# Kernel tuning notes

Hardware: AMD Instinct MI355X
Metric: run time of the kernel (lower is better)

The kernel has to match this reference:

```python
import jax, jax.numpy as jnp
import numpy as np

NEURONS = 512
CHANNELS = 384
H, W = 13, 13
BATCH = 512


def setup_inputs() -> dict:
    key = jax.random.key(0)
    kx, ks, kd, kb = jax.random.split(key, 4)
    x = jax.random.normal(kx, (BATCH, CHANNELS, H, W), dtype=jnp.float32)
    W_s = jax.random.normal(ks, (NEURONS, H, W), dtype=jnp.float32)      # spatial readout per neuron
    W_d = jax.random.normal(kd, (NEURONS, CHANNELS), dtype=jnp.float32)  # channel readout (squeezed 1x1 conv kernel)
    W_b = jax.random.normal(kb, (1, NEURONS), dtype=jnp.float32)
    return {"x": x, "W_s": W_s, "W_d": W_d, "W_b": W_b}


def reference(x, W_s, W_d, W_b):
    # Original: out = einsum('bchw,nhw->bnchw') -> per-neuron 1x1 conv with W_d[n] -> sum over (c,h,w) -> + W_b
    # Mathematically: out[b,n] = sum_{c,h,w} x[b,c,h,w] * W_s[n,h,w] * W_d[n,c] + W_b[0,n]
    # Factorized into two contractions, avoiding the (b,n,c,h,w) intermediate.
    pooled = jnp.einsum('bchw,nhw->bnc', x, W_s)   # spatial weighted pooling: [B, N, C]
    out = jnp.einsum('bnc,nc->bn', pooled, W_d)    # channel readout: [B, N]
    return out + W_b
```

## Files before the change

### kernel.cpp

```cpp
#include <hip/hip_runtime.h>


#define B_   512
#define C_   384
#define N_   512
#define HW_  169
#define CT   128
#define SXR  200
#define RSTR 520

#define WSF_ELEMS  ((size_t)32 * 6 * 64 * 8)
#define WDF_ELEMS  ((size_t)24 * 32 * 64 * 4)
#define PART_ELEMS ((size_t)3 * B_ * N_)

typedef __bf16 bf16x8 __attribute__((ext_vector_type(8)));
typedef float f32x4  __attribute__((ext_vector_type(4)));
typedef float f32x4u __attribute__((ext_vector_type(4), aligned(4)));
typedef unsigned u32x4 __attribute__((ext_vector_type(4)));

__device__ __forceinline__ __bf16 f2bf(float f) {
  union { float f; unsigned u; } v; v.f = f;
  unsigned r = (v.u + 0x7FFFu + ((v.u >> 16) & 1u)) >> 16;
  unsigned short s = (unsigned short)r;
  return __builtin_bit_cast(__bf16, s);
}

__device__ __forceinline__ unsigned pack_trunc(float a, float b) {
  return __builtin_amdgcn_perm(__builtin_bit_cast(unsigned, b),
                               __builtin_bit_cast(unsigned, a), 0x07060302u);
}

__global__ __launch_bounds__(256)
void prep_aux_kernel(const float* __restrict__ Ws,
                     const float* __restrict__ Wd,
                     __bf16* __restrict__ wsf,
                     float* __restrict__ wdf) {
  int t = blockIdx.x * 256 + threadIdx.x;
  if (t < 12288) {
    int lane = t & 63;
    int fr   = t >> 6;
    int kb   = fr % 6;
    int nm   = fr / 6;
    int n    = nm * 16 + (lane & 15);
    int k0   = kb * 32 + (lane >> 4) * 8;
    const float* src = Ws + (size_t)n * HW_;
    bf16x8 v;
    #pragma unroll
    for (int j = 0; j < 8; ++j) {
      int k = k0 + j;
      float f = (k < HW_) ? src[k] : 0.f;
      v[j] = f2bf(f);
    }
    *(bf16x8*)(wsf + (size_t)t * 8) = v;
  } else {
    int t2 = t - 12288;
    int lane = t2 & 63;
    int fr   = t2 >> 6;
    int nm   = fr & 31;
    int cm   = fr >> 5;
    int n    = nm * 16 + (lane & 15);
    int c0   = cm * 16 + (lane >> 4) * 4;
    f32x4 w = *(const f32x4u*)(Wd + (size_t)n * C_ + c0);
    *(f32x4*)(wdf + (size_t)t2 * 4) = w;
  }
}

__global__ __launch_bounds__(256, 4)
void conv_part(const float* __restrict__ x,
               const __bf16* __restrict__ wsf,
               const float* __restrict__ wdf,
               float* __restrict__ part) {
  __shared__ float red[16 * RSTR];

  const int tid  = threadIdx.x;
  const int id    = blockIdx.x;
  const int slot  = id & 7;
  const int t8    = id >> 3;
  const int c_blk = t8 % 3;
  const int b     = (t8 / 3) * 8 + slot;

  const int lane  = tid & 63;
  const int wv    = tid >> 6;
  const int lrow  = lane & 15;
  const int lquad = lane >> 4;

  bf16x8 a[2][6];
  #pragma unroll
  for (int mi = 0; mi < 2; ++mi) {
    const float* rp = x + ((size_t)b * C_ + (size_t)c_blk * CT + wv * 32 + mi * 16 + lrow) * HW_;
    #pragma unroll
    for (int kb = 0; kb < 6; ++kb) {
      const int k0 = kb * 32 + lquad * 8;
      float v0, v1, v2, v3, v4, v5, v6, v7;
      if (kb < 5 || k0 + 7 < HW_) {
        f32x4u t0 = *(const f32x4u*)(rp + k0);
        f32x4u t1 = *(const f32x4u*)(rp + k0 + 4);
        v0 = t0[0]; v1 = t0[1]; v2 = t0[2]; v3 = t0[3];
        v4 = t1[0]; v5 = t1[1]; v6 = t1[2]; v7 = t1[3];
      } else {
        v0 = (k0 + 0 < HW_) ? rp[k0 + 0] : 0.f;
        v1 = v2 = v3 = v4 = v5 = v6 = v7 = 0.f;
      }
      u32x4 pk;
      pk.x = pack_trunc(v0, v1);
      pk.y = pack_trunc(v2, v3);
      pk.z = pack_trunc(v4, v5);
      pk.w = pack_trunc(v6, v7);
      a[mi][kb] = __builtin_bit_cast(bf16x8, pk);
    }
  }

  const int cm0 = c_blk * 8 + wv * 2;
  const __bf16* bb = wsf + (size_t)lane * 8;
  const float*  wb = wdf + (size_t)lane * 4;
  const f32x4 zero = {0.f, 0.f, 0.f, 0.f};
  float* rslot = red + (wv * 4 + lquad) * RSTR + lrow;

  #pragma unroll 1
  for (int nf = 0; nf < 32; ++nf) {
    bf16x8 bfr[6];
    #pragma unroll
    for (int kb = 0; kb < 6; ++kb)
      bfr[kb] = *(const bf16x8*)(bb + ((size_t)nf * 6 + kb) * 512);

    f32x4 acc[2] = {zero, zero};
    #pragma unroll
    for (int kb = 0; kb < 6; ++kb)
      #pragma unroll
      for (int mi = 0; mi < 2; ++mi)
        acc[mi] = __builtin_amdgcn_mfma_f32_16x16x32_bf16(
            a[mi][kb], bfr[kb], acc[mi], 0, 0, 0);

    float t = 0.f;
    #pragma unroll
    for (int mi = 0; mi < 2; ++mi) {
      const f32x4 w = *(const f32x4*)(wb + (((size_t)(cm0 + mi) * 32 + nf) * 256));
      t += acc[mi][0] * w[0] + acc[mi][1] * w[1]
         + acc[mi][2] * w[2] + acc[mi][3] * w[3];
    }
    rslot[nf * 16] = t;
  }
  __syncthreads();

  float* pb = part + ((size_t)c_blk * B_ + b) * N_;
  #pragma unroll
  for (int r = 0; r < 2; ++r) {
    const int n = r * 256 + tid;
    float v = 0.f;
    #pragma unroll
    for (int s = 0; s < 16; ++s)
      v += red[s * RSTR + n];
    pb[n] = v;
  }
}

__global__ __launch_bounds__(256)
void reduce_part(const float* __restrict__ part,
                 const float* __restrict__ Wb,
                 float* __restrict__ out) {
  const size_t S = (size_t)B_ * N_;
  int idx = (blockIdx.x * 256 + threadIdx.x) * 4;
  f32x4 a0 = *(const f32x4u*)(part + idx);
  f32x4 a1 = *(const f32x4u*)(part + S + idx);
  f32x4 a2 = *(const f32x4u*)(part + 2 * S + idx);
  f32x4 wb = *(const f32x4u*)(Wb + (idx & (N_ - 1)));
  f32x4 r;
  #pragma unroll
  for (int i = 0; i < 4; ++i)
    r[i] = a0[i] + a1[i] + a2[i] + wb[i];
  *(f32x4*)(out + idx) = r;
}

__global__ __launch_bounds__(256, 3)
void conv_fused_v8(const float* __restrict__ x,
                   const __bf16* __restrict__ wsf,
                   const float* __restrict__ wdf,
                   const float* __restrict__ Wb,
                   float* __restrict__ out) {
  __shared__ __align__(16) __bf16 Xs[CT * SXR];
  __shared__ float red[4][64];

  const int tid  = threadIdx.x;
  const int id    = blockIdx.x;
  const int slot  = id & 7;
  const int t8    = id >> 3;
  const int c_blk = t8 % 3;
  const int b     = (t8 / 3) * 8 + slot;

  const int lane  = tid & 63;
  const int wv    = tid >> 6;
  const int cq    = (wv >> 1) * 64;
  const int nq    = (wv & 1) * 64;
  const int lrow  = lane & 15;
  const int lquad = lane >> 4;

  const float* src = x + ((size_t)b * C_ + (size_t)c_blk * CT) * HW_;
  #pragma unroll 4
  for (int p = 0; p < 24; ++p) {
    int i   = p * 256 + tid;
    int row = i / 48;
    int ch  = i - row * 48;
    const float* bp = src + row * HW_ + ch * 4;
    float v0 = 0.f, v1 = 0.f, v2 = 0.f, v3 = 0.f;
    if (ch < 42) {
      f32x4u t = *(const f32x4u*)bp;
      v0 = t[0]; v1 = t[1]; v2 = t[2]; v3 = t[3];
    } else if (ch == 42) {
      v0 = bp[0];
    }
    unsigned d0 = pack_trunc(v0, v1);
    unsigned d1 = pack_trunc(v2, v3);
    uint2 d; d.x = d0; d.y = d1;
    *(uint2*)&Xs[row * SXR + ch * 4] = d;
  }
  __syncthreads();

  const int cm0 = c_blk * 8 + (cq >> 4);

  #pragma unroll 1
  for (int nb = 0; nb < 4; ++nb) {
    const int nm0 = nb * 8 + (nq >> 4);
    const __bf16* bbase = wsf + ((size_t)nm0 * 6) * 512 + (size_t)lane * 8;

    const f32x4 zero = {0.f, 0.f, 0.f, 0.f};
    f32x4 acc[4][4];
    #pragma unroll
    for (int mi = 0; mi < 4; ++mi)
      #pragma unroll
      for (int ni = 0; ni < 4; ++ni)
        acc[mi][ni] = zero;

    #pragma unroll
    for (int kb = 0; kb < 6; ++kb) {
      bf16x8 afr[4], bfr[4];
      #pragma unroll
      for (int mi = 0; mi < 4; ++mi)
        afr[mi] = *(const bf16x8*)&Xs[(cq + mi * 16 + lrow) * SXR + kb * 32 + lquad * 8];
      #pragma unroll
      for (int ni = 0; ni < 4; ++ni)
        bfr[ni] = *(const bf16x8*)(bbase + ((size_t)ni * 6 + kb) * 512);
      #pragma unroll
      for (int mi = 0; mi < 4; ++mi)
        #pragma unroll
        for (int ni = 0; ni < 4; ++ni)
          acc[mi][ni] = __builtin_amdgcn_mfma_f32_16x16x32_bf16(
              afr[mi], bfr[ni], acc[mi][ni], 0, 0, 0);
    }

    float s[4] = {0.f, 0.f, 0.f, 0.f};
    #pragma unroll
    for (int ni = 0; ni < 4; ++ni) {
      #pragma unroll
      for (int mi = 0; mi < 4; ++mi) {
        const f32x4 w = *(const f32x4*)(wdf +
            (((size_t)(cm0 + mi) * 32 + (nm0 + ni)) * 64 + lane) * 4);
        s[ni] += acc[mi][ni][0] * w[0] + acc[mi][ni][1] * w[1]
               + acc[mi][ni][2] * w[2] + acc[mi][ni][3] * w[3];
      }
    }

    #pragma unroll
    for (int ni = 0; ni < 4; ++ni) {
      s[ni] += __shfl_xor(s[ni], 16, 64);
      s[ni] += __shfl_xor(s[ni], 32, 64);
    }
    if (lane < 16) {
      #pragma unroll
      for (int ni = 0; ni < 4; ++ni)
        red[wv][ni * 16 + lrow] = s[ni];
    }
    __syncthreads();

    if (tid < 128) {
      const int half = tid >> 6;
      const int idx  = tid & 63;
      const int n    = nb * 128 + tid;
      float v = red[half][idx] + red[half + 2][idx];
      if (c_blk == 0) v += Wb[n];
      atomicAdd(&out[(size_t)b * N_ + n], v);
    }
    __syncthreads();
  }
}


#define LDSS 104
#define KCH  96
#define NT   128

__global__ __launch_bounds__(256)
void conv_main_fallback(const float* __restrict__ x,
                        const float* __restrict__ Ws_g,
                        const float* __restrict__ Wd,
                        const float* __restrict__ Wb,
                        float* __restrict__ out) {
  __shared__ __align__(16) __bf16 Xs[CT][LDSS];
  __shared__ __align__(16) __bf16 Ws[NT][LDSS];

  const int tid   = threadIdx.x;
  const int n_blk = blockIdx.x;
  const int c_blk = blockIdx.y;
  const int b     = blockIdx.z;
  const int c0 = c_blk * CT;
  const int n0 = n_blk * NT;
  const int lane  = tid & 63;
  const int wv    = tid >> 6;
  const int cq    = (wv >> 1) * 64;
  const int nq    = (wv & 1) * 64;
  const int lrow  = lane & 15;
  const int lquad = lane >> 4;

  const f32x4 zero = {0.f, 0.f, 0.f, 0.f};
  f32x4 acc[4][4];
  #pragma unroll
  for (int mi = 0; mi < 4; ++mi)
    #pragma unroll
    for (int ni = 0; ni < 4; ++ni)
      acc[mi][ni] = zero;

  const float* xb  = x    + (size_t)b  * (C_ * HW_) + (size_t)c0 * HW_;
  const float* wsb = Ws_g + (size_t)n0 * HW_;

  for (int ch = 0; ch < 2; ++ch) {
    const int k0 = ch * KCH;
    __syncthreads();
    for (int e = tid; e < CT * KCH; e += 256) {
      int r   = e / KCH;
      int col = e - r * KCH;
      int k   = k0 + col;
      float vx = 0.f, vw = 0.f;
      if (k < HW_) {
        vx = xb [r * HW_ + k];
        vw = wsb[r * HW_ + k];
      }
      Xs[r][col] = f2bf(vx);
      Ws[r][col] = f2bf(vw);
    }
    __syncthreads();

    #pragma unroll
    for (int ks = 0; ks < 3; ++ks) {
      const int kc = ks * 32 + lquad * 8;
      bf16x8 afr[4], bfr[4];
      #pragma unroll
      for (int mi = 0; mi < 4; ++mi)
        afr[mi] = *(const bf16x8*)&Xs[cq + mi * 16 + lrow][kc];
      #pragma unroll
      for (int ni = 0; ni < 4; ++ni)
        bfr[ni] = *(const bf16x8*)&Ws[nq + ni * 16 + lrow][kc];
      #pragma unroll
      for (int mi = 0; mi < 4; ++mi)
        #pragma unroll
        for (int ni = 0; ni < 4; ++ni)
          acc[mi][ni] = __builtin_amdgcn_mfma_f32_16x16x32_bf16(
              afr[mi], bfr[ni], acc[mi][ni], 0, 0, 0);
    }
  }

  #pragma unroll
  for (int ni = 0; ni < 4; ++ni) {
    const int n = n0 + nq + ni * 16 + lrow;
    float sv = 0.f;
    #pragma unroll
    for (int mi = 0; mi < 4; ++mi) {
      const int cbase = c0 + cq + mi * 16 + lquad * 4;
      #pragma unroll
      for (int i = 0; i < 4; ++i)
        sv += acc[mi][ni][i] * Wd[(size_t)n * C_ + (cbase + i)];
    }
    sv += __shfl_xor(sv, 16, 64);
    sv += __shfl_xor(sv, 32, 64);
    if (lane < 16) {
      if (c_blk == 0 && cq == 0) sv += Wb[n];
      atomicAdd(&out[(size_t)b * N_ + n], sv);
    }
  }
}

extern "C" void kernel_launch(void* const* d_in, const int* in_sizes, int n_in,
                              void* d_out, int out_size, void* d_ws, size_t ws_size,
                              hipStream_t stream) {
  const float* x   = (const float*)d_in[0];
  const float* Wsp = (const float*)d_in[1];
  const float* Wd  = (const float*)d_in[2];
  const float* Wb  = (const float*)d_in[3];
  float* out = (float*)d_out;

  const size_t need_basic = WSF_ELEMS * sizeof(__bf16) + WDF_ELEMS * sizeof(float);
  const size_t need_full  = need_basic + PART_ELEMS * sizeof(float);

  if (ws_size >= need_full) {
    __bf16* wsf  = (__bf16*)d_ws;
    float*  wdf  = (float*)(wsf + WSF_ELEMS);
    float*  partb = wdf + WDF_ELEMS;

    prep_aux_kernel<<<240, 256, 0, stream>>>(Wsp, Wd, wsf, wdf);
    conv_part<<<1536, 256, 0, stream>>>(x, wsf, wdf, partb);
    reduce_part<<<256, 256, 0, stream>>>(partb, Wb, out);
  } else if (ws_size >= need_basic) {
    __bf16* wsf = (__bf16*)d_ws;
    float*  wdf = (float*)(wsf + WSF_ELEMS);

    hipMemsetAsync(d_out, 0, (size_t)out_size * sizeof(float), stream);
    prep_aux_kernel<<<240, 256, 0, stream>>>(Wsp, Wd, wsf, wdf);
    conv_fused_v8<<<1536, 256, 0, stream>>>(x, wsf, wdf, Wb, out);
  } else {
    hipMemsetAsync(d_out, 0, (size_t)out_size * sizeof(float), stream);
    dim3 grid(N_ / NT, C_ / CT, B_);
    conv_main_fallback<<<grid, 256, 0, stream>>>(x, Wsp, Wd, Wb, out);
  }
}
```

Measured before the change: 238.1 us.

## Split channel blocks in conv_part to 64 channels, doubling grid and partial sums

Each conv_part block now covers 64 channels instead of 128. Each wave does a single MFMA row tile, so the grid doubles to 3072 blocks and there are six partial-sum slices instead of three. The two quad halves of the accumulator are combined with a shuffle before the LDS store, which halves the shared reduction buffer and raises the occupancy hint. The aim is more parallelism and fewer registers per thread. The cost is that each block re-reads the full Ws/Wd fragments for half the compute, and the reduce kernel has twice the partial traffic.

```diff
diff --git a/kernel.cpp b/kernel.cpp
--- a/kernel.cpp
+++ b/kernel.cpp
@@ -5,13 +5,14 @@
 #define C_   384
 #define N_   512
 #define HW_  169
+#define CT_P 64
 #define CT   128
 #define SXR  200
-#define RSTR 520
+#define RSTR 516
 
 #define WSF_ELEMS  ((size_t)32 * 6 * 64 * 8)
 #define WDF_ELEMS  ((size_t)24 * 32 * 64 * 4)
-#define PART_ELEMS ((size_t)3 * B_ * N_)
+#define PART_ELEMS ((size_t)6 * B_ * N_)
 
 typedef __bf16 bf16x8 __attribute__((ext_vector_type(8)));
 typedef float f32x4  __attribute__((ext_vector_type(4)));
@@ -65,29 +66,28 @@
   }
 }
 
-__global__ __launch_bounds__(256, 4)
+__global__ __launch_bounds__(256, 5)
 void conv_part(const float* __restrict__ x,
                const __bf16* __restrict__ wsf,
                const float* __restrict__ wdf,
                float* __restrict__ part) {
-  __shared__ float red[16 * RSTR];
+  __shared__ float red[8 * RSTR];
 
   const int tid  = threadIdx.x;
   const int id    = blockIdx.x;
   const int slot  = id & 7;
   const int t8    = id >> 3;
-  const int c_blk = t8 % 3;
-  const int b     = (t8 / 3) * 8 + slot;
+  const int c_blk = t8 % 6;
+  const int b     = (t8 / 6) * 8 + slot;
 
   const int lane  = tid & 63;
   const int wv    = tid >> 6;
   const int lrow  = lane & 15;
   const int lquad = lane >> 4;
 
-  bf16x8 a[2][6];
-  #pragma unroll
-  for (int mi = 0; mi < 2; ++mi) {
-    const float* rp = x + ((size_t)b * C_ + (size_t)c_blk * CT + wv * 32 + mi * 16 + lrow) * HW_;
+  bf16x8 a[6];
+  {
+    const float* rp = x + ((size_t)b * C_ + (size_t)c_blk * CT_P + wv * 16 + lrow) * HW_;
     #pragma unroll
     for (int kb = 0; kb < 6; ++kb) {
       const int k0 = kb * 32 + lquad * 8;
@@ -106,15 +106,16 @@
       pk.y = pack_trunc(v2, v3);
       pk.z = pack_trunc(v4, v5);
       pk.w = pack_trunc(v6, v7);
-      a[mi][kb] = __builtin_bit_cast(bf16x8, pk);
-    }
-  }
-
-  const int cm0 = c_blk * 8 + wv * 2;
+      a[kb] = __builtin_bit_cast(bf16x8, pk);
+    }
+  }
+
+  const int cm0 = c_blk * 4 + wv;
   const __bf16* bb = wsf + (size_t)lane * 8;
   const float*  wb = wdf + (size_t)lane * 4;
   const f32x4 zero = {0.f, 0.f, 0.f, 0.f};
-  float* rslot = red + (wv * 4 + lquad) * RSTR + lrow;
+  const int rrow = wv * 2 + (lquad >> 1);
+  const bool wlane = ((lquad & 1) == 0);
 
   #pragma unroll 1
   for (int nf = 0; nf < 32; ++nf) {
@@ -123,22 +124,17 @@
     for (int kb = 0; kb < 6; ++kb)
       bfr[kb] = *(const bf16x8*)(bb + ((size_t)nf * 6 + kb) * 512);
 
-    f32x4 acc[2] = {zero, zero};
+    const f32x4 w = *(const f32x4*)(wb + (((size_t)cm0 * 32 + nf) * 256));
+
+    f32x4 acc = zero;
     #pragma unroll
     for (int kb = 0; kb < 6; ++kb)
-      #pragma unroll
-      for (int mi = 0; mi < 2; ++mi)
-        acc[mi] = __builtin_amdgcn_mfma_f32_16x16x32_bf16(
-            a[mi][kb], bfr[kb], acc[mi], 0, 0, 0);
-
-    float t = 0.f;
-    #pragma unroll
-    for (int mi = 0; mi < 2; ++mi) {
-      const f32x4 w = *(const f32x4*)(wb + (((size_t)(cm0 + mi) * 32 + nf) * 256));
-      t += acc[mi][0] * w[0] + acc[mi][1] * w[1]
-         + acc[mi][2] * w[2] + acc[mi][3] * w[3];
-    }
-    rslot[nf * 16] = t;
+      acc = __builtin_amdgcn_mfma_f32_16x16x32_bf16(a[kb], bfr[kb], acc, 0, 0, 0);
+
+    float t = acc[0] * w[0] + acc[1] * w[1] + acc[2] * w[2] + acc[3] * w[3];
+    t += __shfl_xor(t, 16, 64);
+    if (wlane)
+      red[rrow * RSTR + nf * 16 + lrow] = t;
   }
   __syncthreads();
 
@@ -148,7 +144,7 @@
     const int n = r * 256 + tid;
     float v = 0.f;
     #pragma unroll
-    for (int s = 0; s < 16; ++s)
+    for (int s = 0; s < 8; ++s)
       v += red[s * RSTR + n];
     pb[n] = v;
   }
@@ -160,14 +156,16 @@
                  float* __restrict__ out) {
   const size_t S = (size_t)B_ * N_;
   int idx = (blockIdx.x * 256 + threadIdx.x) * 4;
-  f32x4 a0 = *(const f32x4u*)(part + idx);
-  f32x4 a1 = *(const f32x4u*)(part + S + idx);
-  f32x4 a2 = *(const f32x4u*)(part + 2 * S + idx);
   f32x4 wb = *(const f32x4u*)(Wb + (idx & (N_ - 1)));
   f32x4 r;
   #pragma unroll
-  for (int i = 0; i < 4; ++i)
-    r[i] = a0[i] + a1[i] + a2[i] + wb[i];
+  for (int i = 0; i < 4; ++i) r[i] = wb[i];
+  #pragma unroll
+  for (int s = 0; s < 6; ++s) {
+    f32x4 a = *(const f32x4u*)(part + (size_t)s * S + idx);
+    #pragma unroll
+    for (int i = 0; i < 4; ++i) r[i] += a[i];
+  }
   *(f32x4*)(out + idx) = r;
 }
 
@@ -395,7 +393,7 @@
     float*  partb = wdf + WDF_ELEMS;
 
     prep_aux_kernel<<<240, 256, 0, stream>>>(Wsp, Wd, wsf, wdf);
-    conv_part<<<1536, 256, 0, stream>>>(x, wsf, wdf, partb);
+    conv_part<<<3072, 256, 0, stream>>>(x, wsf, wdf, partb);
     reduce_part<<<256, 256, 0, stream>>>(partb, Wb, out);
   } else if (ws_size >= need_basic) {
     __bf16* wsf = (__bf16*)d_ws;
```

Result: slower. 271.8 us (+14.2%).
